# Performance work log

Measured on AMD Instinct MI355X. Metric: run time of the kernel, lower is better.

## Reference

```python
import math
import jax, jax.numpy as jnp
import numpy as np

N_EMBD = 1024
N_HEAD = 16
B, T = 2, 2048


def _heads(t):
    # (B, T, D) -> (B, H, T, hd)
    b, s, d = t.shape
    return t.reshape(b, s, N_HEAD, d // N_HEAD).transpose(0, 2, 1, 3)


def setup_inputs() -> dict:
    key = jax.random.key(0)
    ks = jax.random.split(key, 7)
    D = N_EMBD
    s = 0.02
    return {
        "x": jax.random.normal(ks[0], (B, T, D), dtype=jnp.float32),
        "w_attn": jax.random.normal(ks[1], (2 * D, D), dtype=jnp.float32) * s,
        "b_attn": jnp.zeros((2 * D,), dtype=jnp.float32),
        "w_k2": jax.random.normal(ks[2], (D, D), dtype=jnp.float32) * s,
        "b_k2": jnp.zeros((D,), dtype=jnp.float32),
        "w_proj": jax.random.normal(ks[3], (D, D), dtype=jnp.float32) * s,
        "b_proj": jnp.zeros((D,), dtype=jnp.float32),
    }


def reference(x, w_attn, b_attn, w_k2, b_k2, w_proj, b_proj):
    b, t, d = x.shape
    hd = d // N_HEAD
    scale = 1.0 / math.sqrt(hd)

    # QKV projections: q,k from c_attn; v is raw x reshaped into heads
    qk = x @ w_attn.T + b_attn
    q, k = jnp.split(qk, 2, axis=-1)
    q, k, v = _heads(q), _heads(k), _heads(x)  # (B,H,T,hd)

    # AR branch: standard causal softmax attention
    scores = jnp.einsum("bhqd,bhkd->bhqk", q, k) * scale
    causal = jnp.tril(jnp.ones((t, t), dtype=bool))
    scores = jnp.where(causal, scores, -jnp.inf)
    y_ar = jnp.einsum("bhqk,bhkd->bhqd", jax.nn.softmax(scores, axis=-1), v)

    # MA branch on one-step residuals e_t = v_{t+1} - y_ar_t
    e = v[:, :, 1:, :] - y_ar[:, :, :-1, :]           # (B,H,T-1,hd)
    q2 = q[:, :, 1:, :]
    k2 = _heads(x[:, :-1] @ w_k2.T + b_k2)            # (B,H,T-1,hd)

    qa = -jax.nn.leaky_relu(-q2 * scale, negative_slope=0.02)  # ma_q_activation
    ka = jax.nn.sigmoid((k2 * scale) * 0.02)                   # ma_k_activation, k=0.02

    ma = jnp.einsum("bhqd,bhkd->bhqk", qa, ka)        # (B,H,T-1,T-1), no softmax
    ma = jnp.where(jnp.tril(jnp.ones((t - 1, t - 1), dtype=bool)), ma, 0.0)
    y_ma = jnp.einsum("bhqk,bhkd->bhqd", ma, e)
    y_ma = jnp.concatenate([jnp.zeros_like(y_ma[:, :, :1, :]), y_ma], axis=2)

    def merge(z):  # (B,H,T,hd) -> (B,T,D)
        return z.transpose(0, 2, 1, 3).reshape(b, t, d)

    out = (merge(y_ar) @ w_proj.T + b_proj) + (merge(y_ma) @ w_proj.T + b_proj)
    return out
```

## Files before the change

kernel.cpp:

```cpp
#include <hip/hip_runtime.h>
#include <hip/hip_bf16.h>
#include <math.h>

#define BB  2
#define TT  2048
#define DDE 1024
#define NHH 16
#define HDD 64

typedef __bf16 bf16_t;
typedef __attribute__((ext_vector_type(8))) __bf16 bf16x8;
typedef __attribute__((ext_vector_type(4))) __bf16 bf16x4;
typedef __attribute__((ext_vector_type(4))) float  f32x4;

#define MFMA(a, b, c) __builtin_amdgcn_mfma_f32_16x16x32_bf16((a), (b), (c), 0, 0, 0)

#define WAIT_VM6()   asm volatile("s_waitcnt vmcnt(6)" ::: "memory")
#define WAIT_VM4()   asm volatile("s_waitcnt vmcnt(4)" ::: "memory")
#define WAIT_VM2()   asm volatile("s_waitcnt vmcnt(2)" ::: "memory")
#define WAIT_VM0()   asm volatile("s_waitcnt vmcnt(0)" ::: "memory")
#define WAIT_LGKM0() asm volatile("s_waitcnt lgkmcnt(0)" ::: "memory")

__device__ inline void wg_barrier() {
    __builtin_amdgcn_sched_barrier(0);
    __builtin_amdgcn_s_barrier();
    __builtin_amdgcn_sched_barrier(0);
}

__device__ inline unsigned int cvtpk(float a, float b) {
    unsigned int r;
    asm("v_cvt_pk_bf16_f32 %0, %1, %2" : "=v"(r) : "v"(a), "v"(b));
    return r;
}

__device__ inline void pl16swap(unsigned int &a, unsigned int &b) {
    asm("v_permlane16_swap_b32 %0, %1" : "+v"(a), "+v"(b));
}

__device__ inline void gll16(const bf16_t* g, unsigned short* l) {
    __builtin_amdgcn_global_load_lds(
        (const __attribute__((address_space(1))) void*)g,
        (__attribute__((address_space(3))) void*)l, 16, 0, 0);
}

template<int ROWS, int NW = 4>
__device__ inline void stage_tile(const bf16_t* g0, size_t gstride,
                                  unsigned short* lds, int wave, int lane)
{
    const int r8 = lane >> 3;
    const int ck = (lane & 7) ^ r8;
    constexpr int RW = ROWS / NW;
    const bf16_t* g = g0 + (size_t)(wave * RW + r8) * gstride + ck * 8;
    unsigned short* l = lds + wave * RW * 64 + lane * 8;
    #pragma unroll
    for (int i = 0; i < RW / 8; ++i)
        gll16(g + (size_t)(i * 8) * gstride, l + i * 512);
}

__global__ __launch_bounds__(256) void cvt_all(
    const float* __restrict__ x, const float* __restrict__ wa,
    const float* __restrict__ wk, const float* __restrict__ wp,
    bf16_t* __restrict__ out)
{
    const size_t NX  = (size_t)BB*TT*DDE;
    const size_t NWA = (size_t)2*DDE*DDE;
    const size_t NW  = (size_t)DDE*DDE;
    const size_t e = ((size_t)blockIdx.x * 256 + threadIdx.x) * 4;
    const float* src;
    if (e < NX)                 src = x  + e;
    else if (e < NX + NWA)      src = wa + (e - NX);
    else if (e < NX + NWA + NW) src = wk + (e - NX - NWA);
    else                        src = wp + (e - NX - NWA - NW);
    float4 v = *(const float4*)src;
    bf16x4 o;
    o[0] = (bf16_t)v.x; o[1] = (bf16_t)v.y;
    o[2] = (bf16_t)v.z; o[3] = (bf16_t)v.w;
    *(bf16x4*)(out + e) = o;
}

__global__ __launch_bounds__(256) void transpose_head(
    const bf16_t* __restrict__ src, bf16_t* __restrict__ dst)
{
    const int t0 = blockIdx.x * 64, h = blockIdx.y, b = blockIdx.z;
    const int tid = threadIdx.x;
    __shared__ __align__(16) bf16_t tile[64 * 64];

    #pragma unroll
    for (int it = 0; it < 2; ++it) {
        const int t = it * 32 + (tid >> 3);
        const int cw = tid & 7;
        const int slot = (cw + (t >> 3)) & 7;
        bf16x8 v = *(const bf16x8*)(src + (size_t)(b*TT + t0 + t)*DDE + h*HDD + cw*8);
        *(bf16x8*)(tile + t*64 + slot*8) = v;
    }
    __syncthreads();
    const int bh = b * NHH + h;
    #pragma unroll
    for (int it = 0; it < 2; ++it) {
        const int d = it * 32 + (tid >> 3);
        const int co = tid & 7;
        const int slot = ((d >> 3) + co) & 7;
        bf16x8 o;
        #pragma unroll
        for (int j = 0; j < 8; ++j)
            o[j] = tile[(co*8 + j)*64 + slot*8 + (d & 7)];
        *(bf16x8*)(dst + (size_t)(bh*64 + d)*TT + t0 + co*8) = o;
    }
}

__global__ __launch_bounds__(256) void build_etg(
    const bf16_t* __restrict__ yarb, const bf16_t* __restrict__ xb,
    bf16_t* __restrict__ etg)
{
    const int t0 = blockIdx.x * 64, h = blockIdx.y, b = blockIdx.z;
    const int tid = threadIdx.x;
    const int bh = b * NHH + h;
    __shared__ __align__(16) bf16_t tile[64 * 64];

    #pragma unroll
    for (int it = 0; it < 2; ++it) {
        const int t = it * 32 + (tid >> 3);
        const int cw = tid & 7;
        const int slot = (cw + (t >> 3)) & 7;
        const int tg = t0 + t;
        bf16x8 ev;
        if (tg == 0) {
            #pragma unroll
            for (int u = 0; u < 8; ++u) ev[u] = (bf16_t)0.f;
        } else {
            bf16x8 xv = *(const bf16x8*)(xb   + (size_t)(b*TT + tg)*DDE + h*HDD + cw*8);
            bf16x8 nv = *(const bf16x8*)(yarb + (size_t)(b*TT + tg - 1)*DDE + h*HDD + cw*8);
            #pragma unroll
            for (int u = 0; u < 8; ++u)
                ev[u] = (bf16_t)((float)xv[u] - (float)nv[u]);
        }
        *(bf16x8*)(tile + t*64 + slot*8) = ev;
    }
    __syncthreads();
    #pragma unroll
    for (int it = 0; it < 2; ++it) {
        const int d = it * 32 + (tid >> 3);
        const int co = tid & 7;
        const int slot = ((d >> 3) + co) & 7;
        bf16x8 o;
        #pragma unroll
        for (int j = 0; j < 8; ++j)
            o[j] = tile[(co*8 + j)*64 + slot*8 + (d & 7)];
        *(bf16x8*)(etg + (size_t)(bh*64 + d)*TT + t0 + co*8) = o;
    }
}

__global__ __launch_bounds__(256) void gemm_qkk2(
    const bf16_t* __restrict__ A, const bf16_t* __restrict__ wab,
    const bf16_t* __restrict__ wkb, const float* __restrict__ b_attn,
    const float* __restrict__ b_k2, bf16_t* __restrict__ qkb,
    bf16_t* __restrict__ qab, bf16_t* __restrict__ kcs)
{
    __shared__ __align__(16) unsigned short As[2][64 * 64];
    __shared__ __align__(16) unsigned short Bs[2][128 * 64];
    const int tid  = threadIdx.x;
    const int wave = tid >> 6, lane = tid & 63;
    const int l15  = lane & 15, quad = lane >> 4;
    const int lid = (int)blockIdx.y * 24 + (int)blockIdx.x;
    const int s   = (lid & 7) * 192 + (lid >> 3);
    const int bm = (s / 24) * 64, bn = (s % 24) * 128;
    const int wm = (wave & 1) * 32, wn = (wave >> 1) * 64;
    const int region = bn >> 10;
    const int K = DDE;
    constexpr int NST = DDE / 64;

    const bf16_t* W = (region < 2) ? wab + (size_t)bn * K
                                   : wkb + (size_t)(bn - 2048) * K;
    const float* bp = (region < 2) ? b_attn + bn : b_k2 + (bn - 2048);
    const bf16_t* Ab = A + (size_t)bm * K;

    f32x4 acc[2][4];
    #pragma unroll
    for (int i = 0; i < 2; ++i)
        #pragma unroll
        for (int j = 0; j < 4; ++j) acc[i][j] = (f32x4)0.f;

    stage_tile<64>(Ab, K, As[0], wave, lane);
    stage_tile<128>(W,  K, Bs[0], wave, lane);
    stage_tile<64>(Ab + 64, K, As[1], wave, lane);
    stage_tile<128>(W  + 64, K, Bs[1], wave, lane);

    for (int t = 0; t < NST; ++t) {
        if (t + 1 < NST) WAIT_VM6(); else WAIT_VM0();
        wg_barrier();
        const unsigned short* Ac = As[t & 1];
        const unsigned short* Bc = Bs[t & 1];
        bf16x8 af[2][2], bfr[4][2];
        #pragma unroll
        for (int mt = 0; mt < 2; ++mt)
            #pragma unroll
            for (int kh = 0; kh < 2; ++kh)
                af[mt][kh] = *(const bf16x8*)(Ac + (wm + mt*16 + l15)*64
                                              + (((kh*4 + quad) ^ (l15 & 7))*8));
        #pragma unroll
        for (int nt = 0; nt < 4; ++nt)
            #pragma unroll
            for (int kh = 0; kh < 2; ++kh)
                bfr[nt][kh] = *(const bf16x8*)(Bc + (wn + nt*16 + l15)*64
                                               + (((kh*4 + quad) ^ (l15 & 7))*8));
        __builtin_amdgcn_s_setprio(1);
        #pragma unroll
        for (int mt = 0; mt < 2; ++mt)
            #pragma unroll
            for (int nt = 0; nt < 4; ++nt) {
                acc[mt][nt] = MFMA(af[mt][0], bfr[nt][0], acc[mt][nt]);
                acc[mt][nt] = MFMA(af[mt][1], bfr[nt][1], acc[mt][nt]);
            }
        __builtin_amdgcn_s_setprio(0);
        WAIT_LGKM0();
        wg_barrier();
        if (t + 2 < NST) {
            stage_tile<64>(Ab + (t+2)*64, K, As[t & 1], wave, lane);
            stage_tile<128>(W  + (t+2)*64, K, Bs[t & 1], wave, lane);
        }
    }

    #pragma unroll
    for (int nt = 0; nt < 4; ++nt) {
        const int cl = wn + nt*16 + l15;
        const float bj = bp[cl];
        const int cg = bn + cl;
        #pragma unroll
        for (int mt = 0; mt < 2; ++mt)
            #pragma unroll
            for (int r = 0; r < 4; ++r) {
                const int row = bm + wm + mt*16 + quad*4 + r;
                const float v = acc[mt][nt][r] + bj;
                if (region == 0) {
                    qkb[(size_t)row * (2*DDE) + cg] = (bf16_t)(v * 0.180336880f);
                    const float z = v * 0.125f;
                    qab[(size_t)row * DDE + cg] = (bf16_t)((v > 0.f) ? 0.02f*z : z);
                } else if (region == 1) {
                    qkb[(size_t)row * (2*DDE) + cg] = (bf16_t)v;
                } else {
                    const int c2 = cg - 2048;
                    const float kc = 1.f/(1.f + __expf(-v*0.0025f)) - 0.5f;
                    if (((row + 1) & (TT - 1)) != 0)
                        kcs[(size_t)(row + 1) * DDE + c2] = (bf16_t)kc;
                    if ((row & (TT - 1)) == 0)
                        kcs[(size_t)row * DDE + c2] = (bf16_t)0.f;
                }
            }
    }
}

__global__ __launch_bounds__(256) void gemm_proj(
    const bf16_t* __restrict__ A, const bf16_t* __restrict__ W,
    const float* __restrict__ bias, float* __restrict__ C,
    int M, int N, int K, float bmul)
{
    __shared__ __align__(16) unsigned short As[2][64 * 64];
    __shared__ __align__(16) unsigned short Bs[2][64 * 64];
    const int tid  = threadIdx.x;
    const int wave = tid >> 6, lane = tid & 63;
    const int l15  = lane & 15, quad = lane >> 4;
    const int lid = (int)blockIdx.y * 16 + (int)blockIdx.x;
    const int s   = (lid & 7) * 128 + (lid >> 3);
    const int bm = (s / 16) * 64, bn = (s % 16) * 64;
    const int wm = (wave & 1) * 32, wn = (wave >> 1) * 32;

    const bf16_t* Ab = A + (size_t)bm * K;
    const bf16_t* Wb = W + (size_t)bn * K;
    const int NST = K / 64;

    f32x4 acc[2][2];
    #pragma unroll
    for (int i = 0; i < 2; ++i)
        #pragma unroll
        for (int j = 0; j < 2; ++j) acc[i][j] = (f32x4)0.f;

    stage_tile<64>(Ab, K, As[0], wave, lane);
    stage_tile<64>(Wb, K, Bs[0], wave, lane);
    stage_tile<64>(Ab + 64, K, As[1], wave, lane);
    stage_tile<64>(Wb + 64, K, Bs[1], wave, lane);

    for (int t = 0; t < NST; ++t) {
        if (t + 1 < NST) WAIT_VM4(); else WAIT_VM0();
        wg_barrier();
        const unsigned short* Ac = As[t & 1];
        const unsigned short* Bc = Bs[t & 1];
        bf16x8 af[2][2], bfr[2][2];
        #pragma unroll
        for (int mt = 0; mt < 2; ++mt)
            #pragma unroll
            for (int kh = 0; kh < 2; ++kh)
                af[mt][kh] = *(const bf16x8*)(Ac + (wm + mt*16 + l15)*64
                                              + (((kh*4 + quad) ^ (l15 & 7))*8));
        #pragma unroll
        for (int nt = 0; nt < 2; ++nt)
            #pragma unroll
            for (int kh = 0; kh < 2; ++kh)
                bfr[nt][kh] = *(const bf16x8*)(Bc + (wn + nt*16 + l15)*64
                                               + (((kh*4 + quad) ^ (l15 & 7))*8));
        __builtin_amdgcn_s_setprio(1);
        #pragma unroll
        for (int mt = 0; mt < 2; ++mt)
            #pragma unroll
            for (int nt = 0; nt < 2; ++nt) {
                acc[mt][nt] = MFMA(af[mt][0], bfr[nt][0], acc[mt][nt]);
                acc[mt][nt] = MFMA(af[mt][1], bfr[nt][1], acc[mt][nt]);
            }
        __builtin_amdgcn_s_setprio(0);
        WAIT_LGKM0();
        wg_barrier();
        if (t + 2 < NST) {
            stage_tile<64>(Ab + (t+2)*64, K, As[t & 1], wave, lane);
            stage_tile<64>(Wb + (t+2)*64, K, Bs[t & 1], wave, lane);
        }
    }

    #pragma unroll
    for (int nt = 0; nt < 2; ++nt) {
        const int col = bn + wn + nt*16 + l15;
        const float bj = bias[col] * bmul;
        #pragma unroll
        for (int mt = 0; mt < 2; ++mt)
            #pragma unroll
            for (int r = 0; r < 4; ++r) {
                const int row = bm + wm + mt*16 + quad*4 + r;
                C[(size_t)row * N + col] = acc[mt][nt][r] + bj;
            }
    }
}

__global__ __launch_bounds__(512) void attn_ar_mfma(
    const bf16_t* __restrict__ qkb, const bf16_t* __restrict__ vtg,
    bf16_t* __restrict__ yarb)
{
    const int h = blockIdx.y, b = blockIdx.z;
    const int p = b ? (15 - (int)blockIdx.x) : (int)blockIdx.x;
    const int qtL = p, qtH = 31 - p;
    const int tid = threadIdx.x, wave = tid >> 6, lane = tid & 63;
    const int l15 = lane & 15, quad = lane >> 4;
    const int qt = (wave < 4) ? qtL : qtH;
    const int qw0 = qt * 64 + (wave & 3) * 16;
    const int bh = b * NHH + h;

    __shared__ __align__(16) unsigned short Ks[2][64 * 64];
    __shared__ __align__(16) unsigned short Vs[2][64 * 64];

    const int nit = qtH + 1;

    const bf16_t* kg = qkb + (size_t)(b*TT)*(2*DDE) + DDE + h*HDD;
    const bf16_t* vg = vtg + (size_t)(bh*64)*TT;

    const bf16_t* qrow = qkb + (size_t)(b*TT + qw0 + l15)*(2*DDE) + h*HDD;
    bf16x8 qf[2];
    qf[0] = *(const bf16x8*)(qrow + quad*8);
    qf[1] = *(const bf16x8*)(qrow + (quad + 4)*8);

    stage_tile<64, 8>(kg, 2*DDE, Ks[0], wave, lane);
    stage_tile<64, 8>(vg, TT, Vs[0], wave, lane);
    stage_tile<64, 8>(kg + (size_t)64*(2*DDE), 2*DDE, Ks[1], wave, lane);
    stage_tile<64, 8>(vg + 64, TT, Vs[1], wave, lane);
    WAIT_VM2();
    wg_barrier();

    f32x4 o[4];
    f32x4 ls = (f32x4)0.f;
    #pragma unroll
    for (int nt = 0; nt < 4; ++nt) o[nt] = (f32x4)0.f;
    bf16x8 onesb;
    #pragma unroll
    for (int j = 0; j < 8; ++j) onesb[j] = (bf16_t)1.f;

    const int cq = ((quad & 1) << 1) | (quad >> 1);

    for (int it = 0; it < nit; ++it) {
        if (it > 0) {
            if (it + 1 < nit) WAIT_VM2(); else WAIT_VM0();
            wg_barrier();
        }
        const int s0 = it * 64;
        const unsigned short* Kc = Ks[it & 1];
        const unsigned short* Vc = Vs[it & 1];

        if (s0 <= qw0 + 31) {
            f32x4 sv[4];
            __builtin_amdgcn_s_setprio(1);
            #pragma unroll
            for (int nt = 0; nt < 4; ++nt) {
                const unsigned short* kr = Kc + (nt*16 + l15)*64;
                bf16x8 kb0 = *(const bf16x8*)(kr + ((quad    ) ^ (l15 & 7))*8);
                bf16x8 kb1 = *(const bf16x8*)(kr + ((quad + 4) ^ (l15 & 7))*8);
                f32x4 z = (f32x4)0.f;
                z = MFMA(kb0, qf[0], z);
                z = MFMA(kb1, qf[1], z);
                sv[nt] = z;
            }
            __builtin_amdgcn_s_setprio(0);

            const bool domask = (s0 + 63 > qw0);
            const int qg = qw0 + l15;
            unsigned int pk[4][2];
            #pragma unroll
            for (int nt = 0; nt < 4; ++nt) {
                float pv[4];
                #pragma unroll
                for (int r = 0; r < 4; ++r) {
                    float pe = exp2f(sv[nt][r]);
                    if (domask) {
                        const int sg = s0 + nt*16 + quad*4 + r;
                        if (sg > qg) pe = 0.f;
                    }
                    pv[r] = pe;
                }
                pk[nt][0] = cvtpk(pv[0], pv[1]);
                pk[nt][1] = cvtpk(pv[2], pv[3]);
            }
            bf16x8 pa[2];
            #pragma unroll
            for (int sc = 0; sc < 2; ++sc) {
                pl16swap(pk[2*sc][0], pk[2*sc+1][0]);
                pl16swap(pk[2*sc][1], pk[2*sc+1][1]);
                union { unsigned int u[4]; bf16x8 v; } pu;
                pu.u[0] = pk[2*sc][0];
                pu.u[1] = pk[2*sc][1];
                pu.u[2] = pk[2*sc+1][0];
                pu.u[3] = pk[2*sc+1][1];
                pa[sc] = pu.v;
            }

            __builtin_amdgcn_s_setprio(1);
            ls = MFMA(pa[0], onesb, ls);
            ls = MFMA(pa[1], onesb, ls);
            #pragma unroll
            for (int nt = 0; nt < 4; ++nt) {
                const unsigned short* vr = Vc + (nt*16 + l15)*64;
                bf16x8 vb0 = *(const bf16x8*)(vr + ((cq    ) ^ (l15 & 7))*8);
                bf16x8 vb1 = *(const bf16x8*)(vr + ((cq + 4) ^ (l15 & 7))*8);
                o[nt] = MFMA(pa[0], vb0, o[nt]);
                o[nt] = MFMA(pa[1], vb1, o[nt]);
            }
            __builtin_amdgcn_s_setprio(0);
        }
        WAIT_LGKM0();
        wg_barrier();
        if (it + 2 < nit) {
            stage_tile<64, 8>(kg + (size_t)(it+2)*64*(2*DDE), 2*DDE, Ks[it & 1], wave, lane);
            stage_tile<64, 8>(vg + (it+2)*64, TT, Vs[it & 1], wave, lane);
        }
    }

    float inv[4];
    #pragma unroll
    for (int r = 0; r < 4; ++r) inv[r] = 1.f / ls[r];
    #pragma unroll
    for (int nt = 0; nt < 4; ++nt)
        #pragma unroll
        for (int r = 0; r < 4; ++r) {
            const int row = qw0 + quad*4 + r;
            const int col = h*HDD + nt*16 + l15;
            yarb[(size_t)(b*TT + row)*DDE + col] = (bf16_t)(o[nt][r] * inv[r]);
        }
}

__global__ __launch_bounds__(512) void attn_ma_mfma(
    const bf16_t* __restrict__ qab, const bf16_t* __restrict__ kcs,
    const bf16_t* __restrict__ etg, const bf16_t* __restrict__ yarb,
    bf16_t* __restrict__ ysumb)
{
    const int h = blockIdx.y, b = blockIdx.z;
    const int p = b ? (15 - (int)blockIdx.x) : (int)blockIdx.x;
    const int qtL = p, qtH = 31 - p;
    const int tid = threadIdx.x, wave = tid >> 6, lane = tid & 63;
    const int l15 = lane & 15, quad = lane >> 4;
    const int qt = (wave < 4) ? qtL : qtH;
    const int qw0 = qt * 64 + (wave & 3) * 16;
    const int bh = b * NHH + h;

    __shared__ __align__(16) unsigned short Ks[2][64 * 64];
    __shared__ __align__(16) unsigned short Es[2][64 * 64];

    const int nit = qtH + 1;

    const bf16_t* kg = kcs + (size_t)(b*TT)*DDE + h*HDD;
    const bf16_t* eg = etg + (size_t)(bh*64)*TT;

    const bf16_t* qrow = qab + (size_t)(b*TT + qw0 + l15)*DDE + h*HDD;
    bf16x8 qf[2];
    qf[0] = *(const bf16x8*)(qrow + quad*8);
    qf[1] = *(const bf16x8*)(qrow + (quad + 4)*8);

    stage_tile<64, 8>(kg, DDE, Ks[0], wave, lane);
    stage_tile<64, 8>(eg, TT, Es[0], wave, lane);
    stage_tile<64, 8>(kg + (size_t)64*DDE, DDE, Ks[1], wave, lane);
    stage_tile<64, 8>(eg + 64, TT, Es[1], wave, lane);
    WAIT_VM2();
    wg_barrier();

    float rs = 0.f;
    #pragma unroll
    for (int kc = 0; kc < 2; ++kc)
        #pragma unroll
        for (int u = 0; u < 8; ++u) rs += (float)qf[kc][u];
    rs += __shfl_xor(rs, 16);
    rs += __shfl_xor(rs, 32);
    const float Rr = 0.5f * rs;

    f32x4 o[4];
    #pragma unroll
    for (int nt = 0; nt < 4; ++nt) o[nt] = (f32x4)0.f;

    const int cq = ((quad & 1) << 1) | (quad >> 1);

    for (int it = 0; it < nit; ++it) {
        if (it > 0) {
            if (it + 1 < nit) WAIT_VM2(); else WAIT_VM0();
            wg_barrier();
        }
        const int s0 = it * 64;
        const unsigned short* Kc = Ks[it & 1];
        const unsigned short* Ec = Es[it & 1];

        if (s0 <= qw0 + 31) {
            f32x4 sv[4];
            __builtin_amdgcn_s_setprio(1);
            #pragma unroll
            for (int nt = 0; nt < 4; ++nt) {
                const unsigned short* kr = Kc + (nt*16 + l15)*64;
                bf16x8 kb0 = *(const bf16x8*)(kr + ((quad    ) ^ (l15 & 7))*8);
                bf16x8 kb1 = *(const bf16x8*)(kr + ((quad + 4) ^ (l15 & 7))*8);
                f32x4 z = (f32x4)0.f;
                z = MFMA(kb0, qf[0], z);
                z = MFMA(kb1, qf[1], z);
                sv[nt] = z;
            }
            __builtin_amdgcn_s_setprio(0);

            const bool domask = (s0 + 63 > qw0);
            const bool m0 = (it == 0);
            const int qg = qw0 + l15;
            unsigned int pk[4][2];
            #pragma unroll
            for (int nt = 0; nt < 4; ++nt) {
                float pv[4];
                #pragma unroll
                for (int r = 0; r < 4; ++r) {
                    const int sg = s0 + nt*16 + quad*4 + r;
                    float pe = sv[nt][r] + Rr;
                    if (m0 && sg == 0) pe = 0.f;
                    if (domask && sg > qg) pe = 0.f;
                    pv[r] = pe;
                }
                pk[nt][0] = cvtpk(pv[0], pv[1]);
                pk[nt][1] = cvtpk(pv[2], pv[3]);
            }
            bf16x8 pa[2];
            #pragma unroll
            for (int sc = 0; sc < 2; ++sc) {
                pl16swap(pk[2*sc][0], pk[2*sc+1][0]);
                pl16swap(pk[2*sc][1], pk[2*sc+1][1]);
                union { unsigned int u[4]; bf16x8 v; } pu;
                pu.u[0] = pk[2*sc][0];
                pu.u[1] = pk[2*sc][1];
                pu.u[2] = pk[2*sc+1][0];
                pu.u[3] = pk[2*sc+1][1];
                pa[sc] = pu.v;
            }

            __builtin_amdgcn_s_setprio(1);
            #pragma unroll
            for (int nt = 0; nt < 4; ++nt) {
                const unsigned short* er = Ec + (nt*16 + l15)*64;
                bf16x8 eb0 = *(const bf16x8*)(er + ((cq    ) ^ (l15 & 7))*8);
                bf16x8 eb1 = *(const bf16x8*)(er + ((cq + 4) ^ (l15 & 7))*8);
                o[nt] = MFMA(pa[0], eb0, o[nt]);
                o[nt] = MFMA(pa[1], eb1, o[nt]);
            }
            __builtin_amdgcn_s_setprio(0);
        }
        WAIT_LGKM0();
        wg_barrier();
        if (it + 2 < nit) {
            stage_tile<64, 8>(kg + (size_t)(it+2)*64*DDE, DDE, Ks[it & 1], wave, lane);
            stage_tile<64, 8>(eg + (it+2)*64, TT, Es[it & 1], wave, lane);
        }
    }

    #pragma unroll
    for (int nt = 0; nt < 4; ++nt)
        #pragma unroll
        for (int r = 0; r < 4; ++r) {
            const int row = qw0 + quad*4 + r;
            const int col = h*HDD + nt*16 + l15;
            const size_t e = (size_t)(b*TT + row)*DDE + col;
            ysumb[e] = (bf16_t)((float)yarb[e] + o[nt][r]);
        }
}

extern "C" void kernel_launch(void* const* d_in, const int* in_sizes, int n_in,
                              void* d_out, int out_size, void* d_ws, size_t ws_size,
                              hipStream_t stream)
{
    const float* x      = (const float*)d_in[0];
    const float* w_attn = (const float*)d_in[1];
    const float* b_attn = (const float*)d_in[2];
    const float* w_k2   = (const float*)d_in[3];
    const float* b_k2   = (const float*)d_in[4];
    const float* w_proj = (const float*)d_in[5];
    const float* b_proj = (const float*)d_in[6];

    const size_t NX  = (size_t)BB*TT*DDE;
    const size_t NWA = (size_t)2*DDE*DDE;
    const size_t NW  = (size_t)DDE*DDE;
    const size_t NQK = (size_t)BB*TT*2*DDE;

    bf16_t* xb   = (bf16_t*)d_ws;
    bf16_t* wab  = xb   + NX;
    bf16_t* wkb  = wab  + NWA;
    bf16_t* wpb  = wkb  + NW;
    bf16_t* qkb  = wpb  + NW;
    bf16_t* qab  = qkb  + NQK;
    bf16_t* kcs  = qab  + NX;
    bf16_t* vtg  = kcs  + NX;
    bf16_t* ysumb= vtg  + NX;
    bf16_t* yarb = (bf16_t*)((float*)(vtg + NX) + NX);
    bf16_t* etg  = vtg;

    const size_t NCVT = NX + NWA + NW + NW;
    cvt_all<<<NCVT / 1024, 256, 0, stream>>>(x, w_attn, w_k2, w_proj, xb);

    transpose_head<<<dim3(TT/64, NHH, BB), 256, 0, stream>>>(xb, vtg);

    const int M = BB * TT;
    gemm_qkk2<<<dim3(24, M/64), 256, 0, stream>>>(xb, wab, wkb, b_attn, b_k2,
                                                   qkb, qab, kcs);

    attn_ar_mfma<<<dim3(16, NHH, BB), 512, 0, stream>>>(qkb, vtg, yarb);
    build_etg<<<dim3(TT/64, NHH, BB), 256, 0, stream>>>(yarb, xb, etg);
    attn_ma_mfma<<<dim3(16, NHH, BB), 512, 0, stream>>>(qab, kcs, etg, yarb, ysumb);

    gemm_proj<<<dim3(DDE/64, M/64), 256, 0, stream>>>(ysumb, wpb, b_proj,
                                                      (float*)d_out, M, DDE, DDE, 2.f);
}
```

Before: 240.1 us.

## Process KV tiles in pairs per barrier with deeper double-buffered staging

```diff
diff --git a/kernel.cpp b/kernel.cpp
--- a/kernel.cpp
+++ b/kernel.cpp
@@ -17,7 +17,6 @@
 
 #define WAIT_VM6()   asm volatile("s_waitcnt vmcnt(6)" ::: "memory")
 #define WAIT_VM4()   asm volatile("s_waitcnt vmcnt(4)" ::: "memory")
-#define WAIT_VM2()   asm volatile("s_waitcnt vmcnt(2)" ::: "memory")
 #define WAIT_VM0()   asm volatile("s_waitcnt vmcnt(0)" ::: "memory")
 #define WAIT_LGKM0() asm volatile("s_waitcnt lgkmcnt(0)" ::: "memory")
 
@@ -30,6 +29,12 @@
 __device__ inline unsigned int cvtpk(float a, float b) {
     unsigned int r;
     asm("v_cvt_pk_bf16_f32 %0, %1, %2" : "=v"(r) : "v"(a), "v"(b));
+    return r;
+}
+
+__device__ inline float fexp2(float x) {
+    float r;
+    asm("v_exp_f32 %0, %1" : "=v"(r) : "v"(x));
     return r;
 }
 
@@ -341,10 +346,11 @@
     const int qw0 = qt * 64 + (wave & 3) * 16;
     const int bh = b * NHH + h;
 
-    __shared__ __align__(16) unsigned short Ks[2][64 * 64];
-    __shared__ __align__(16) unsigned short Vs[2][64 * 64];
+    __shared__ __align__(16) unsigned short Ks[2][2][64 * 64];
+    __shared__ __align__(16) unsigned short Vs[2][2][64 * 64];
 
     const int nit = qtH + 1;
+    const int npair = (nit + 1) >> 1;
 
     const bf16_t* kg = qkb + (size_t)(b*TT)*(2*DDE) + DDE + h*HDD;
     const bf16_t* vg = vtg + (size_t)(bh*64)*TT;
@@ -354,11 +360,18 @@
     qf[0] = *(const bf16x8*)(qrow + quad*8);
     qf[1] = *(const bf16x8*)(qrow + (quad + 4)*8);
 
-    stage_tile<64, 8>(kg, 2*DDE, Ks[0], wave, lane);
-    stage_tile<64, 8>(vg, TT, Vs[0], wave, lane);
-    stage_tile<64, 8>(kg + (size_t)64*(2*DDE), 2*DDE, Ks[1], wave, lane);
-    stage_tile<64, 8>(vg + 64, TT, Vs[1], wave, lane);
-    WAIT_VM2();
+    stage_tile<64, 8>(kg, 2*DDE, Ks[0][0], wave, lane);
+    stage_tile<64, 8>(vg, TT, Vs[0][0], wave, lane);
+    stage_tile<64, 8>(kg + (size_t)64*(2*DDE), 2*DDE, Ks[0][1], wave, lane);
+    stage_tile<64, 8>(vg + 64, TT, Vs[0][1], wave, lane);
+    {
+        const int t2 = min(2, nit-1), t3 = min(3, nit-1);
+        stage_tile<64, 8>(kg + (size_t)t2*64*(2*DDE), 2*DDE, Ks[1][0], wave, lane);
+        stage_tile<64, 8>(vg + t2*64, TT, Vs[1][0], wave, lane);
+        stage_tile<64, 8>(kg + (size_t)t3*64*(2*DDE), 2*DDE, Ks[1][1], wave, lane);
+        stage_tile<64, 8>(vg + t3*64, TT, Vs[1][1], wave, lane);
+    }
+    WAIT_VM4();
     wg_barrier();
 
     f32x4 o[4];
@@ -371,79 +384,87 @@
 
     const int cq = ((quad & 1) << 1) | (quad >> 1);
 
-    for (int it = 0; it < nit; ++it) {
-        if (it > 0) {
-            if (it + 1 < nit) WAIT_VM2(); else WAIT_VM0();
+    for (int jp = 0; jp < npair; ++jp) {
+        if (jp > 0) {
+            if (jp + 1 < npair) WAIT_VM4(); else WAIT_VM0();
             wg_barrier();
         }
-        const int s0 = it * 64;
-        const unsigned short* Kc = Ks[it & 1];
-        const unsigned short* Vc = Vs[it & 1];
-
-        if (s0 <= qw0 + 31) {
-            f32x4 sv[4];
-            __builtin_amdgcn_s_setprio(1);
-            #pragma unroll
-            for (int nt = 0; nt < 4; ++nt) {
-                const unsigned short* kr = Kc + (nt*16 + l15)*64;
-                bf16x8 kb0 = *(const bf16x8*)(kr + ((quad    ) ^ (l15 & 7))*8);
-                bf16x8 kb1 = *(const bf16x8*)(kr + ((quad + 4) ^ (l15 & 7))*8);
-                f32x4 z = (f32x4)0.f;
-                z = MFMA(kb0, qf[0], z);
-                z = MFMA(kb1, qf[1], z);
-                sv[nt] = z;
+        #pragma unroll
+        for (int half = 0; half < 2; ++half) {
+            const int tt = 2*jp + half;
+            const int s0 = tt * 64;
+            if (tt < nit && s0 <= qw0 + 31) {
+                const unsigned short* Kc = Ks[jp & 1][half];
+                const unsigned short* Vc = Vs[jp & 1][half];
+
+                f32x4 sv[4];
+                __builtin_amdgcn_s_setprio(1);
+                #pragma unroll
+                for (int nt = 0; nt < 4; ++nt) {
+                    const unsigned short* kr = Kc + (nt*16 + l15)*64;
+                    bf16x8 kb0 = *(const bf16x8*)(kr + ((quad    ) ^ (l15 & 7))*8);
+                    bf16x8 kb1 = *(const bf16x8*)(kr + ((quad + 4) ^ (l15 & 7))*8);
+                    f32x4 z = (f32x4)0.f;
+                    z = MFMA(kb0, qf[0], z);
+                    z = MFMA(kb1, qf[1], z);
+                    sv[nt] = z;
+                }
+                __builtin_amdgcn_s_setprio(0);
+
+                const bool domask = (s0 + 63 > qw0);
+                const int qg = qw0 + l15;
+                unsigned int pk[4][2];
+                #pragma unroll
+                for (int nt = 0; nt < 4; ++nt) {
+                    float pv[4];
+                    #pragma unroll
+                    for (int r = 0; r < 4; ++r) {
+                        float pe = fexp2(sv[nt][r]);
+                        if (domask) {
+                            const int sg = s0 + nt*16 + quad*4 + r;
+                            if (sg > qg) pe = 0.f;
+                        }
+                        pv[r] = pe;
+                    }
+                    pk[nt][0] = cvtpk(pv[0], pv[1]);
+                    pk[nt][1] = cvtpk(pv[2], pv[3]);
+                }
+                bf16x8 pa[2];
+                #pragma unroll
+                for (int sc = 0; sc < 2; ++sc) {
+                    pl16swap(pk[2*sc][0], pk[2*sc+1][0]);
+                    pl16swap(pk[2*sc][1], pk[2*sc+1][1]);
+                    union { unsigned int u[4]; bf16x8 v; } pu;
+                    pu.u[0] = pk[2*sc][0];
+                    pu.u[1] = pk[2*sc][1];
+                    pu.u[2] = pk[2*sc+1][0];
+                    pu.u[3] = pk[2*sc+1][1];
+                    pa[sc] = pu.v;
+                }
+
+                __builtin_amdgcn_s_setprio(1);
+                ls = MFMA(pa[0], onesb, ls);
+                ls = MFMA(pa[1], onesb, ls);
+                #pragma unroll
+                for (int nt = 0; nt < 4; ++nt) {
+                    const unsigned short* vr = Vc + (nt*16 + l15)*64;
+                    bf16x8 vb0 = *(const bf16x8*)(vr + ((cq    ) ^ (l15 & 7))*8);
+                    bf16x8 vb1 = *(const bf16x8*)(vr + ((cq + 4) ^ (l15 & 7))*8);
+                    o[nt] = MFMA(pa[0], vb0, o[nt]);
+                    o[nt] = MFMA(pa[1], vb1, o[nt]);
+                }
+                __builtin_amdgcn_s_setprio(0);
             }
-            __builtin_amdgcn_s_setprio(0);
-
-            const bool domask = (s0 + 63 > qw0);
-            const int qg = qw0 + l15;
-            unsigned int pk[4][2];
-            #pragma unroll
-            for (int nt = 0; nt < 4; ++nt) {
-                float pv[4];
-                #pragma unroll
-                for (int r = 0; r < 4; ++r) {
-                    float pe = exp2f(sv[nt][r]);
-                    if (domask) {
-                        const int sg = s0 + nt*16 + quad*4 + r;
-                        if (sg > qg) pe = 0.f;
-                    }
-                    pv[r] = pe;
-                }
-                pk[nt][0] = cvtpk(pv[0], pv[1]);
-                pk[nt][1] = cvtpk(pv[2], pv[3]);
-            }
-            bf16x8 pa[2];
-            #pragma unroll
-            for (int sc = 0; sc < 2; ++sc) {
-                pl16swap(pk[2*sc][0], pk[2*sc+1][0]);
-                pl16swap(pk[2*sc][1], pk[2*sc+1][1]);
-                union { unsigned int u[4]; bf16x8 v; } pu;
-                pu.u[0] = pk[2*sc][0];
-                pu.u[1] = pk[2*sc][1];
-                pu.u[2] = pk[2*sc+1][0];
-                pu.u[3] = pk[2*sc+1][1];
-                pa[sc] = pu.v;
-            }
-
-            __builtin_amdgcn_s_setprio(1);
-            ls = MFMA(pa[0], onesb, ls);
-            ls = MFMA(pa[1], onesb, ls);
-            #pragma unroll
-            for (int nt = 0; nt < 4; ++nt) {
-                const unsigned short* vr = Vc + (nt*16 + l15)*64;
-                bf16x8 vb0 = *(const bf16x8*)(vr + ((cq    ) ^ (l15 & 7))*8);
-                bf16x8 vb1 = *(const bf16x8*)(vr + ((cq + 4) ^ (l15 & 7))*8);
-                o[nt] = MFMA(pa[0], vb0, o[nt]);
-                o[nt] = MFMA(pa[1], vb1, o[nt]);
-            }
-            __builtin_amdgcn_s_setprio(0);
         }
         WAIT_LGKM0();
         wg_barrier();
-        if (it + 2 < nit) {
-            stage_tile<64, 8>(kg + (size_t)(it+2)*64*(2*DDE), 2*DDE, Ks[it & 1], wave, lane);
-            stage_tile<64, 8>(vg + (it+2)*64, TT, Vs[it & 1], wave, lane);
+        if (jp + 2 < npair) {
+            const int t0 = 2*(jp + 2);
+            const int t1 = min(t0 + 1, nit - 1);
+            stage_tile<64, 8>(kg + (size_t)t0*64*(2*DDE), 2*DDE, Ks[jp & 1][0], wave, lane);
+            stage_tile<64, 8>(vg + t0*64, TT, Vs[jp & 1][0], wave, lane);
+            stage_tile<64, 8>(kg + (size_t)t1*64*(2*DDE), 2*DDE, Ks[jp & 1][1], wave, lane);
+            stage_tile<64, 8>(vg + t1*64, TT, Vs[jp & 1][1], wave, lane);
         }
     }
 
@@ -474,10 +495,11 @@
     const int qw0 = qt * 64 + (wave & 3) * 16;
     const int bh = b * NHH + h;
 
-    __shared__ __align__(16) unsigned short Ks[2][64 * 64];
-    __shared__ __align__(16) unsigned short Es[2][64 * 64];
+    __shared__ __align__(16) unsigned short Ks[2][2][64 * 64];
+    __shared__ __align__(16) unsigned short Es[2][2][64 * 64];
 
     const int nit = qtH + 1;
+    const int npair = (nit + 1) >> 1;
 
     const bf16_t* kg = kcs + (size_t)(b*TT)*DDE + h*HDD;
     const bf16_t* eg = etg + (size_t)(bh*64)*TT;
@@ -487,11 +509,18 @@
     qf[0] = *(const bf16x8*)(qrow + quad*8);
     qf[1] = *(const bf16x8*)(qrow + (quad + 4)*8);
 
-    stage_tile<64, 8>(kg, DDE, Ks[0], wave, lane);
-    stage_tile<64, 8>(eg, TT, Es[0], wave, lane);
-    stage_tile<64, 8>(kg + (size_t)64*DDE, DDE, Ks[1], wave, lane);
-    stage_tile<64, 8>(eg + 64, TT, Es[1], wave, lane);
-    WAIT_VM2();
+    stage_tile<64, 8>(kg, DDE, Ks[0][0], wave, lane);
+    stage_tile<64, 8>(eg, TT, Es[0][0], wave, lane);
+    stage_tile<64, 8>(kg + (size_t)64*DDE, DDE, Ks[0][1], wave, lane);
+    stage_tile<64, 8>(eg + 64, TT, Es[0][1], wave, lane);
+    {
+        const int t2 = min(2, nit-1), t3 = min(3, nit-1);
+        stage_tile<64, 8>(kg + (size_t)t2*64*DDE, DDE, Ks[1][0], wave, lane);
+        stage_tile<64, 8>(eg + t2*64, TT, Es[1][0], wave, lane);
+        stage_tile<64, 8>(kg + (size_t)t3*64*DDE, DDE, Ks[1][1], wave, lane);
+        stage_tile<64, 8>(eg + t3*64, TT, Es[1][1], wave, lane);
+    }
+    WAIT_VM4();
     wg_barrier();
 
     float rs = 0.f;
@@ -509,77 +538,85 @@
 
     const int cq = ((quad & 1) << 1) | (quad >> 1);
 
-    for (int it = 0; it < nit; ++it) {
-        if (it > 0) {
-            if (it + 1 < nit) WAIT_VM2(); else WAIT_VM0();
+    for (int jp = 0; jp < npair; ++jp) {
+        if (jp > 0) {
+            if (jp + 1 < npair) WAIT_VM4(); else WAIT_VM0();
             wg_barrier();
         }
-        const int s0 = it * 64;
-        const unsigned short* Kc = Ks[it & 1];
-        const unsigned short* Ec = Es[it & 1];
-
-        if (s0 <= qw0 + 31) {
-            f32x4 sv[4];
-            __builtin_amdgcn_s_setprio(1);
-            #pragma unroll
-            for (int nt = 0; nt < 4; ++nt) {
-                const unsigned short* kr = Kc + (nt*16 + l15)*64;
-                bf16x8 kb0 = *(const bf16x8*)(kr + ((quad    ) ^ (l15 & 7))*8);
-                bf16x8 kb1 = *(const bf16x8*)(kr + ((quad + 4) ^ (l15 & 7))*8);
-                f32x4 z = (f32x4)0.f;
-                z = MFMA(kb0, qf[0], z);
-                z = MFMA(kb1, qf[1], z);
-                sv[nt] = z;
+        #pragma unroll
+        for (int half = 0; half < 2; ++half) {
+            const int tt = 2*jp + half;
+            const int s0 = tt * 64;
+            if (tt < nit && s0 <= qw0 + 31) {
+                const unsigned short* Kc = Ks[jp & 1][half];
+                const unsigned short* Ec = Es[jp & 1][half];
+
+                f32x4 sv[4];
+                __builtin_amdgcn_s_setprio(1);
+                #pragma unroll
+                for (int nt = 0; nt < 4; ++nt) {
+                    const unsigned short* kr = Kc + (nt*16 + l15)*64;
+                    bf16x8 kb0 = *(const bf16x8*)(kr + ((quad    ) ^ (l15 & 7))*8);
+                    bf16x8 kb1 = *(const bf16x8*)(kr + ((quad + 4) ^ (l15 & 7))*8);
+                    f32x4 z = (f32x4)0.f;
+                    z = MFMA(kb0, qf[0], z);
+                    z = MFMA(kb1, qf[1], z);
+                    sv[nt] = z;
+                }
+                __builtin_amdgcn_s_setprio(0);
+
+                const bool domask = (s0 + 63 > qw0);
+                const bool m0 = (tt == 0);
+                const int qg = qw0 + l15;
+                unsigned int pk[4][2];
+                #pragma unroll
+                for (int nt = 0; nt < 4; ++nt) {
+                    float pv[4];
+                    #pragma unroll
+                    for (int r = 0; r < 4; ++r) {
+                        const int sg = s0 + nt*16 + quad*4 + r;
+                        float pe = sv[nt][r] + Rr;
+                        if (m0 && sg == 0) pe = 0.f;
+                        if (domask && sg > qg) pe = 0.f;
+                        pv[r] = pe;
+                    }
+                    pk[nt][0] = cvtpk(pv[0], pv[1]);
+                    pk[nt][1] = cvtpk(pv[2], pv[3]);
+                }
+                bf16x8 pa[2];
+                #pragma unroll
+                for (int sc = 0; sc < 2; ++sc) {
+                    pl16swap(pk[2*sc][0], pk[2*sc+1][0]);
+                    pl16swap(pk[2*sc][1], pk[2*sc+1][1]);
+                    union { unsigned int u[4]; bf16x8 v; } pu;
+                    pu.u[0] = pk[2*sc][0];
+                    pu.u[1] = pk[2*sc][1];
+                    pu.u[2] = pk[2*sc+1][0];
+                    pu.u[3] = pk[2*sc+1][1];
+                    pa[sc] = pu.v;
+                }
+
+                __builtin_amdgcn_s_setprio(1);
+                #pragma unroll
+                for (int nt = 0; nt < 4; ++nt) {
+                    const unsigned short* er = Ec + (nt*16 + l15)*64;
+                    bf16x8 eb0 = *(const bf16x8*)(er + ((cq    ) ^ (l15 & 7))*8);
+                    bf16x8 eb1 = *(const bf16x8*)(er + ((cq + 4) ^ (l15 & 7))*8);
+                    o[nt] = MFMA(pa[0], eb0, o[nt]);
+                    o[nt] = MFMA(pa[1], eb1, o[nt]);
+                }
+                __builtin_amdgcn_s_setprio(0);
             }
-            __builtin_amdgcn_s_setprio(0);
-
-            const bool domask = (s0 + 63 > qw0);
-            const bool m0 = (it == 0);
-            const int qg = qw0 + l15;
-            unsigned int pk[4][2];
-            #pragma unroll
-            for (int nt = 0; nt < 4; ++nt) {
-                float pv[4];
-                #pragma unroll
-                for (int r = 0; r < 4; ++r) {
-                    const int sg = s0 + nt*16 + quad*4 + r;
-                    float pe = sv[nt][r] + Rr;
-                    if (m0 && sg == 0) pe = 0.f;
-                    if (domask && sg > qg) pe = 0.f;
-                    pv[r] = pe;
-                }
-                pk[nt][0] = cvtpk(pv[0], pv[1]);
-                pk[nt][1] = cvtpk(pv[2], pv[3]);
-            }
-            bf16x8 pa[2];
-            #pragma unroll
-            for (int sc = 0; sc < 2; ++sc) {
-                pl16swap(pk[2*sc][0], pk[2*sc+1][0]);
-                pl16swap(pk[2*sc][1], pk[2*sc+1][1]);
-                union { unsigned int u[4]; bf16x8 v; } pu;
-                pu.u[0] = pk[2*sc][0];
-                pu.u[1] = pk[2*sc][1];
-                pu.u[2] = pk[2*sc+1][0];
-                pu.u[3] = pk[2*sc+1][1];
-                pa[sc] = pu.v;
-            }
-
-            __builtin_amdgcn_s_setprio(1);
-            #pragma unroll
-            for (int nt = 0; nt < 4; ++nt) {
-                const unsigned short* er = Ec + (nt*16 + l15)*64;
-                bf16x8 eb0 = *(const bf16x8*)(er + ((cq    ) ^ (l15 & 7))*8);
-                bf16x8 eb1 = *(const bf16x8*)(er + ((cq + 4) ^ (l15 & 7))*8);
-                o[nt] = MFMA(pa[0], eb0, o[nt]);
-                o[nt] = MFMA(pa[1], eb1, o[nt]);
-            }
-            __builtin_amdgcn_s_setprio(0);
         }
         WAIT_LGKM0();
         wg_barrier();
-        if (it + 2 < nit) {
-            stage_tile<64, 8>(kg + (size_t)(it+2)*64*DDE, DDE, Ks[it & 1], wave, lane);
-            stage_tile<64, 8>(eg + (it+2)*64, TT, Es[it & 1], wave, lane);
+        if (jp + 2 < npair) {
+            const int t0 = 2*(jp + 2);
+            const int t1 = min(t0 + 1, nit - 1);
+            stage_tile<64, 8>(kg + (size_t)t0*64*DDE, DDE, Ks[jp & 1][0], wave, lane);
+            stage_tile<64, 8>(eg + t0*64, TT, Es[jp & 1][0], wave, lane);
+            stage_tile<64, 8>(kg + (size_t)t1*64*DDE, DDE, Ks[jp & 1][1], wave, lane);
+            stage_tile<64, 8>(eg + t1*64, TT, Es[jp & 1][1], wave, lane);
         }
     }
 
```

New measurement: 229.3 us. -4.5%, faster.
